# Performance work log

Hardware: AMD Instinct MI355X
Metric: run time of the kernel (lower is better)

## Reference

```python
import jax, jax.numpy as jnp
import numpy as np
from jax import lax

B, N, T, H, V, C = 256, 196, 26, 512, 12000, 1000


def setup_inputs() -> dict:
    key = jax.random.key(0)
    ks = jax.random.split(key, 24)
    g = lambda i, shape, s=0.02: jax.random.normal(ks[i], shape, jnp.float32) * s
    z = lambda *shape: jnp.zeros(shape, jnp.float32)
    return {
        "image": jax.random.normal(ks[0], (B, N, H), jnp.float32),
        "question": jax.random.randint(ks[1], (B, T), 0, V, jnp.int32),
        "embed_table": g(2, (V, H), 1.0),
        "W_img": g(3, (H, H)), "b_img": z(H),
        "W_uni": g(4, (1, H, H)), "b_uni": z(H),
        "W_bi": g(5, (2, H, H)), "b_bi": z(H),
        "W_tri": g(6, (3, H, H)), "b_tri": z(H),
        "lstm_k": g(7, (H, 4 * H)), "lstm_rk": g(8, (H, 4 * H)), "lstm_b": z(4 * H),
        "W_corr": g(9, (H, H)), "b_corr": z(H),
        "W_qe": g(10, (H, H)), "b_qe": z(H),
        "W_ie": g(11, (H, H)), "b_ie": z(H),
        "w_qa": g(12, (H, 1)), "b_qa": z(1),
        "w_ia": g(13, (H, 1)), "b_ia": z(1),
        "W_w": g(14, (H, H)), "b_w": z(H),
        "W_p": g(15, (2 * H, H)), "b_p": z(H),
        "W_s": g(16, (2 * H, H)), "b_s": z(H),
        "W_fc1": g(17, (H, 2 * H)), "b_fc1": z(2 * H),
        "W_fc": g(18, (2 * H, C)), "b_fc": z(C),
    }


def _conv1d(x, w, b, dil):
    # x: [B,T,H], w: [k, in, out] (WIO). TF 'same' padding == XLA SAME.
    y = lax.conv_general_dilated(x, w, window_strides=(1,), padding='SAME',
                                 rhs_dilation=(dil,),
                                 dimension_numbers=('NWC', 'WIO', 'NWC'))
    return y + b


def _lstm(x, k, rk, b):
    # Keras LSTM, gate order i,f,c,o; inference (dropout off).
    xp = jnp.einsum('bth,hg->btg', x, k) + b  # [B,T,4H]
    h0 = jnp.zeros((x.shape[0], rk.shape[0]), x.dtype)

    def step(carry, xt):
        h, c = carry
        zg = xt + h @ rk
        i, f, g, o = jnp.split(zg, 4, axis=-1)
        i, f, o = jax.nn.sigmoid(i), jax.nn.sigmoid(f), jax.nn.sigmoid(o)
        c = f * c + i * jnp.tanh(g)
        h = o * jnp.tanh(c)
        return (h, c), h

    _, hs = lax.scan(step, (h0, h0), jnp.swapaxes(xp, 0, 1))
    return jnp.swapaxes(hs, 0, 1)  # [B,T,H]


def _co_attention(img_feat, ques_feat, W_corr, b_corr, W_qe, b_qe, W_ie, b_ie,
                  w_qa, b_qa, w_ia, b_ia):
    img_corr = img_feat @ W_corr + b_corr                       # [B,N,H]
    wm = jnp.tanh(jnp.einsum('btd,bnd->btn', ques_feat, img_corr))  # affinity
    ques_embed = ques_feat @ W_qe + b_qe                        # [B,T,H]
    img_embed = img_feat @ W_ie + b_ie                          # [B,N,H]
    ques_sum = jnp.tanh(jnp.einsum('btn,bnd->btd', wm, img_embed) + ques_embed)
    ques_att = jax.nn.softmax((ques_sum @ w_qa + b_qa)[..., 0], axis=-1)  # [B,T]
    img_sum = jnp.tanh(jnp.einsum('btn,btd->bnd', wm, ques_embed) + img_embed)
    img_att = jax.nn.softmax((img_sum @ w_ia + b_ia)[..., 0], axis=-1)    # [B,N]
    q_feat = jnp.einsum('bt,btd->bd', ques_att, ques_feat)
    v_feat = jnp.einsum('bn,bnd->bd', img_att, img_feat)
    return v_feat, q_feat


def reference(image, question, embed_table, W_img, b_img, W_uni, b_uni, W_bi, b_bi,
              W_tri, b_tri, lstm_k, lstm_rk, lstm_b, W_corr, b_corr, W_qe, b_qe,
              W_ie, b_ie, w_qa, b_qa, w_ia, b_ia, W_w, b_w, W_p, b_p, W_s, b_s,
              W_fc1, b_fc1, W_fc, b_fc):
    img = jnp.tanh(image @ W_img + b_img)                       # [B,N,H]
    words = embed_table[question]                               # [B,T,H]
    uni = jnp.tanh(_conv1d(words, W_uni, b_uni, 1))
    bi = jnp.tanh(_conv1d(words, W_bi, b_bi, 2))
    tri = jnp.tanh(_conv1d(words, W_tri, b_tri, 2))
    phrase = jnp.tanh(jnp.maximum(jnp.maximum(uni, bi), tri))   # maxpool over 3 n-grams
    sentence = _lstm(phrase, lstm_k, lstm_rk, lstm_b)
    ca = lambda v, q: _co_attention(v, q, W_corr, b_corr, W_qe, b_qe, W_ie, b_ie,
                                    w_qa, b_qa, w_ia, b_ia)
    v_word, q_word = ca(img, words)
    v_phr, q_phr = ca(img, phrase)
    v_sent, q_sent = ca(img, sentence)
    h_w = jnp.tanh((q_word + v_word) @ W_w + b_w)
    h_p = jnp.tanh(jnp.concatenate([q_phr + v_phr, h_w], axis=1) @ W_p + b_p)
    h_s = jnp.tanh(jnp.concatenate([q_sent + v_sent, h_p], axis=1) @ W_s + b_s)
    fc1 = jax.nn.relu(h_s @ W_fc1 + b_fc1)
    return jax.nn.softmax(fc1 @ W_fc + b_fc, axis=-1)           # [B,C]
```

## Files before the change

kernel.cpp:

```cpp
#include <hip/hip_runtime.h>
#include <hip/hip_bf16.h>
#include <math.h>

#define Bq   256
#define Nimg 196
#define Tseq 26
#define Hd   512
#define H4   2048
#define Ccls 1000
#define KP   1536
#define MT3  19968

typedef int   int4v  __attribute__((ext_vector_type(4)));
typedef float f32x4  __attribute__((ext_vector_type(4)));

#define SWZ8(x) ((x) ^ (((x) >> 3) & 7))

__device__ __forceinline__ float fast_tanh(float x) {
    float e = __expf(2.0f * x);
    return 1.0f - 2.0f * __builtin_amdgcn_rcpf(e + 1.0f);
}
__device__ __forceinline__ float fast_sigmoid(float x) {
    return __builtin_amdgcn_rcpf(1.0f + __expf(-x));
}

__device__ __forceinline__ short f2bf(float x) {
    union { float f; unsigned u; } a; a.f = x;
    unsigned r = a.u + 0x7FFF + ((a.u >> 16) & 1);
    return (short)(r >> 16);
}
__device__ __forceinline__ float bf2f(short b) {
    union { float f; unsigned u; } a; a.u = ((unsigned)(unsigned short)b) << 16;
    return a.f;
}

__global__ void embed_kernel(const int* __restrict__ q, const float* __restrict__ table,
                             short* __restrict__ words2) {
    int row = blockIdx.x;
    int tok = q[row];
    int c4 = threadIdx.x * 4;
    float4 v = *reinterpret_cast<const float4*>(table + (size_t)tok * Hd + c4);
    short h0 = f2bf(v.x), h1 = f2bf(v.y), h2 = f2bf(v.z), h3 = f2bf(v.w);
    short l0 = f2bf(v.x - bf2f(h0)), l1 = f2bf(v.y - bf2f(h1));
    short l2 = f2bf(v.z - bf2f(h2)), l3 = f2bf(v.w - bf2f(h3));
    *reinterpret_cast<short4*>(words2 + (size_t)row * 1024 + c4) = make_short4(h0, h1, h2, h3);
    *reinterpret_cast<short4*>(words2 + (size_t)row * 1024 + 512 + c4) = make_short4(l0, l1, l2, l3);
}

__global__ void split_kernel(const float* __restrict__ X, short* __restrict__ X2) {
    int i4 = blockIdx.x * 256 + threadIdx.x;
    int m = i4 >> 7, c4 = (i4 & 127) * 4;
    float4 v = *reinterpret_cast<const float4*>(X + ((size_t)m << 9) + c4);
    short h0 = f2bf(v.x), h1 = f2bf(v.y), h2 = f2bf(v.z), h3 = f2bf(v.w);
    short l0 = f2bf(v.x - bf2f(h0)), l1 = f2bf(v.y - bf2f(h1));
    short l2 = f2bf(v.z - bf2f(h2)), l3 = f2bf(v.w - bf2f(h3));
    *reinterpret_cast<short4*>(X2 + (size_t)m * 1024 + c4) = make_short4(h0, h1, h2, h3);
    *reinterpret_cast<short4*>(X2 + (size_t)m * 1024 + 512 + c4) = make_short4(l0, l1, l2, l3);
}

__global__ __launch_bounds__(256) void wsplit_all_kernel(
    const float* __restrict__ W_img, const float* __restrict__ W_corr,
    const float* __restrict__ W_ie, const float* __restrict__ W_qe,
    const float* __restrict__ W_uni, const float* __restrict__ W_bi,
    const float* __restrict__ W_tri, const float* __restrict__ lstm_k,
    short* __restrict__ WimgT2, short* __restrict__ WcorrR2,
    short* __restrict__ WieT2, short* __restrict__ WqeT2,
    short* __restrict__ WconvT2, short* __restrict__ lkT2) {
    const int z = blockIdx.z;
    const int tid = threadIdx.x;
    const int k0 = blockIdx.y * 64;
    const size_t HK = (size_t)Hd * KP;
    if (z == 1) {
        const int n0 = blockIdx.x * 64;
        const int n = tid >> 2, ksub = (tid & 3) * 16;
        const float* src = W_corr + (size_t)(n0 + n) * Hd + k0 + ksub;
        size_t base = (size_t)(n0 + n) * KP + k0 + ksub;
        #pragma unroll
        for (int k = 0; k < 16; ++k) {
            float x = src[k];
            short h = f2bf(x);
            short l = f2bf(x - bf2f(h));
            WcorrR2[base + k] = h;
            WcorrR2[base + 512 + k] = h;
            WcorrR2[base + 1024 + k] = l;
        }
        return;
    }
    const float* W; short* WT2; int Nw, n0;
    if (z < 10) {
        Nw = Hd; n0 = blockIdx.x * 64;
        switch (z) {
            case 0: W = W_img;  WT2 = WimgT2;  break;
            case 2: W = W_ie;   WT2 = WieT2;   break;
            case 3: W = W_qe;   WT2 = WqeT2;   break;
            case 4: W = W_uni;                     WT2 = WconvT2 + 0 * HK; break;
            case 5: W = W_bi;                      WT2 = WconvT2 + 1 * HK; break;
            case 6: W = W_bi + (size_t)Hd * Hd;    WT2 = WconvT2 + 2 * HK; break;
            case 7: W = W_tri;                     WT2 = WconvT2 + 3 * HK; break;
            case 8: W = W_tri + (size_t)Hd * Hd;   WT2 = WconvT2 + 4 * HK; break;
            default:W = W_tri + 2 * (size_t)Hd * Hd; WT2 = WconvT2 + 5 * HK; break;
        }
    } else {
        Nw = H4; W = lstm_k; WT2 = lkT2;
        n0 = ((z - 10) * 8 + blockIdx.x) * 64;
    }
    __shared__ float tile[64][65];
    #pragma unroll
    for (int p = 0; p < 16; ++p) {
        int r = p * 4 + (tid >> 6);
        int c = tid & 63;
        tile[r][c] = W[(size_t)(k0 + r) * Nw + n0 + c];
    }
    __syncthreads();
    const int n = tid >> 2;
    const int ksub = (tid & 3) * 16;
    size_t base = (size_t)(n0 + n) * KP + k0 + ksub;
    #pragma unroll
    for (int k = 0; k < 16; ++k) {
        float x = tile[ksub + k][n];
        short h = f2bf(x);
        short l = f2bf(x - bf2f(h));
        WT2[base + k] = h;
        WT2[base + 512 + k] = h;
        WT2[base + 1024 + k] = l;
    }
}

__global__ __launch_bounds__(256) void qb_kernel(const short* __restrict__ Q2,
                                                 const float* __restrict__ b_corr,
                                                 float* __restrict__ qb) {
    const int tid = threadIdx.x, lane = tid & 63, wid = tid >> 6;
    const int r = blockIdx.x * 4 + wid;
    const short* row = Q2 + (size_t)r * 1024 + lane * 8;
    float v = 0.f;
    #pragma unroll
    for (int k = 0; k < 8; ++k) {
        float x = bf2f(row[k]) + bf2f(row[512 + k]);
        v += x * b_corr[lane * 8 + k];
    }
    #pragma unroll
    for (int off = 32; off; off >>= 1) v += __shfl_xor(v, off);
    if (lane == 0) qb[r] = v;
}

__device__ __forceinline__ void mfma16(f32x4& acc, int4v a, int4v b) {
    asm volatile("v_mfma_f32_16x16x32_bf16 %0, %1, %2, %0" : "+v"(acc) : "v"(a), "v"(b));
}

template <int ACT, int OUT>
__global__ __launch_bounds__(512) void mfma_gemm8_kernel(
    const short* __restrict__ A2, const short* __restrict__ W2T,
    const float* __restrict__ bias, float* __restrict__ C, short* __restrict__ C2,
    int M, int N) {
    __shared__ __align__(16) short L[2][2][4][4096];
    const int tid = threadIdx.x;
    const int lane = tid & 63, wid = tid >> 6;
    const int Cn = N >> 8;
    const int nwg = (M >> 8) * Cn;
    int Lb = blockIdx.x;
    int xcd = Lb & 7, lq = Lb >> 3;
    int q8 = nwg >> 3, r8 = nwg & 7;
    int logical = (xcd < r8 ? xcd * (q8 + 1) : r8 * (q8 + 1) + (xcd - r8) * q8) + lq;
    const int row0 = (logical / Cn) << 8, col0 = (logical % Cn) << 8;
    const int wm = wid >> 2, wn = wid & 3;
    const int sdec = SWZ8(tid);
    const int frs = sdec >> 6, rs = (sdec >> 2) & 15, kb = sdec & 3;
    const int koff = kb * 8;
    const int aro = frs * 16 + rs;
    const short* aptr[2]; const short* bptr[2];
    aptr[0] = A2 + (size_t)(row0 + aro) * 1024;
    aptr[1] = A2 + (size_t)(row0 + 128 + aro) * 1024;
    bptr[0] = W2T + (size_t)(col0 + aro) * KP;
    bptr[1] = W2T + (size_t)(col0 + 128 + aro) * KP;
    const int ldso = wid * 64 * 8;
    auto STAGE = [&](int slot, int tile, int p) {
        int h = p & 1, kh = p >> 1;
        int kk = tile * 64 + kh * 32 + koff;
        int ka = kk >= 1024 ? kk - 1024 : kk;
        __builtin_amdgcn_global_load_lds(
            (const __attribute__((address_space(1))) void*)(aptr[h] + ka),
            (__attribute__((address_space(3))) void*)(&L[slot][0][h * 2 + kh][ldso]),
            16, 0, 0);
        __builtin_amdgcn_global_load_lds(
            (const __attribute__((address_space(1))) void*)(bptr[h] + kk),
            (__attribute__((address_space(3))) void*)(&L[slot][1][h * 2 + kh][ldso]),
            16, 0, 0);
    };
    f32x4 acc[8][4] = {};
    #pragma unroll
    for (int p = 0; p < 4; ++p) STAGE(0, 0, p);
    const int NT = KP / 64;
    for (int t = 0; t < NT; ++t) {
        const int sl = t & 1;
        int4v bfr[4][2];
        #pragma unroll
        for (int p = 0; p < 4; ++p) {
            if (p == 0) {
                if (t + 1 < NT) {
                    STAGE(sl ^ 1, t + 1, 0);
                    asm volatile("s_waitcnt vmcnt(2)" ::: "memory");
                } else {
                    asm volatile("s_waitcnt vmcnt(0)" ::: "memory");
                }
                __builtin_amdgcn_s_barrier();
                __builtin_amdgcn_sched_barrier(0);
                #pragma unroll
                for (int nf = 0; nf < 4; ++nf)
                    #pragma unroll
                    for (int kh = 0; kh < 2; ++kh) {
                        int off = ((wn & 1) * 4 + nf) * 64 + (lane & 15) * 4 + (lane >> 4);
                        bfr[nf][kh] = *reinterpret_cast<const int4v*>(
                            &L[sl][1][(wn >> 1) * 2 + kh][SWZ8(off) * 8]);
                    }
            } else {
                if (t + 1 < NT) STAGE(sl ^ 1, t + 1, p);
            }
            int4v af[2][2];
            #pragma unroll
            for (int i = 0; i < 2; ++i)
                #pragma unroll
                for (int kh = 0; kh < 2; ++kh) {
                    int off = (p * 2 + i) * 64 + (lane & 15) * 4 + (lane >> 4);
                    af[i][kh] = *reinterpret_cast<const int4v*>(
                        &L[sl][0][wm * 2 + kh][SWZ8(off) * 8]);
                }
            __builtin_amdgcn_s_setprio(1);
            #pragma unroll
            for (int i = 0; i < 2; ++i)
                #pragma unroll
                for (int nf = 0; nf < 4; ++nf)
                    #pragma unroll
                    for (int kh = 0; kh < 2; ++kh)
                        mfma16(acc[p * 2 + i][nf], af[i][kh], bfr[nf][kh]);
            __builtin_amdgcn_s_setprio(0);
        }
        asm volatile("s_waitcnt lgkmcnt(0)" ::: "memory");
        __builtin_amdgcn_s_barrier();
        __builtin_amdgcn_sched_barrier(0);
    }
    asm volatile("s_nop 7\n\ts_nop 7" ::: "memory");
    #pragma unroll
    for (int mf = 0; mf < 8; ++mf) {
        #pragma unroll
        for (int nf = 0; nf < 4; ++nf) {
            int col = col0 + wn * 64 + nf * 16 + (lane & 15);
            float bv;
            if (OUT == 2) bv = (col >= 512) ? bias[col - 512] : 0.f;
            else bv = bias ? bias[col] : 0.f;
            #pragma unroll
            for (int r = 0; r < 4; ++r) {
                int row = row0 + wm * 128 + mf * 16 + (lane >> 4) * 4 + r;
                float v = acc[mf][nf][r] + bv;
                if (ACT == 1) v = fast_tanh(v);
                if (OUT == 0) {
                    C[(size_t)row * N + col] = v;
                } else if (OUT == 1) {
                    short h = f2bf(v), l = f2bf(v - bf2f(h));
                    C2[(size_t)row * 1024 + col] = h;
                    C2[(size_t)row * 1024 + 512 + col] = l;
                } else {
                    if (col < 512) {
                        short h = f2bf(v), l = f2bf(v - bf2f(h));
                        C2[(size_t)row * 1024 + col] = h;
                        C2[(size_t)row * 1024 + 512 + col] = l;
                    } else {
                        C[(size_t)row * Hd + (col - 512)] = v;
                    }
                }
            }
        }
    }
}

__global__ __launch_bounds__(256) void wm3_mfma_kernel(
    const short* __restrict__ Qc2, const short* __restrict__ img2,
    const float* __restrict__ qb, float* __restrict__ wm0, float* __restrict__ wm1,
    float* __restrict__ wm2) {
    __shared__ __align__(16) short Asl[2][4096];
    __shared__ __align__(16) short Bsl[2][4096];
    const int tid = threadIdx.x;
    const int lane = tid & 63, wid = tid >> 6;
    const int col0 = blockIdx.x * 128;
    const int b = blockIdx.y;
    const int wmq = wid >> 1, wn = wid & 1;
    const short* ab[2]; const short* bb[2]; int koff[2];
    #pragma unroll
    for (int c = 0; c < 2; ++c) {
        int d = c * 256 + tid;
        int s = SWZ8(d);
        int fr = s >> 6, r = (s >> 2) & 15, kb = s & 3;
        koff[c] = kb * 8;
        int arow = fr * 16 + r;
        int lvl = arow / 26, at = arow - lvl * 26;
        if (arow >= 78) { lvl = 0; at = 0; }
        ab[c] = Qc2 + ((size_t)lvl * (Bq * Tseq) + (size_t)(b * 26 + at)) * 1024;
        int brow = col0 + fr * 16 + r;
        if (brow > 195) brow = 195;
        bb[c] = img2 + ((size_t)(b * 196 + brow)) * 1024;
    }
    auto STAGE = [&](int buf, int k0) {
        #pragma unroll
        for (int c = 0; c < 2; ++c) {
            int kk = k0 + koff[c];
            int ka = kk >= 1024 ? kk - 1024 : kk;
            int kbv = kk >= 512 ? kk - 512 : kk;
            __builtin_amdgcn_global_load_lds(
                (const __attribute__((address_space(1))) void*)(ab[c] + ka),
                (__attribute__((address_space(3))) void*)(&Asl[buf][(c * 256 + wid * 64) * 8]),
                16, 0, 0);
            __builtin_amdgcn_global_load_lds(
                (const __attribute__((address_space(1))) void*)(bb[c] + kbv),
                (__attribute__((address_space(3))) void*)(&Bsl[buf][(c * 256 + wid * 64) * 8]),
                16, 0, 0);
        }
    };
    f32x4 acc[4][4] = {};
    STAGE(0, 0);
    int cur = 0;
    for (int k0 = 0; k0 < KP; k0 += 32) {
        if (k0 + 32 < KP) {
            STAGE(cur ^ 1, k0 + 32);
            asm volatile("s_waitcnt vmcnt(4)" ::: "memory");
        } else {
            asm volatile("s_waitcnt vmcnt(0)" ::: "memory");
        }
        __builtin_amdgcn_s_barrier();
        __builtin_amdgcn_sched_barrier(0);
        int4v af[4], bfr[4];
        #pragma unroll
        for (int f = 0; f < 4; ++f) {
            int sa = (wmq * 4 + f) * 64 + (lane & 15) * 4 + (lane >> 4);
            af[f] = *reinterpret_cast<const int4v*>(&Asl[cur][SWZ8(sa) * 8]);
            int sb = (wn * 4 + f) * 64 + (lane & 15) * 4 + (lane >> 4);
            bfr[f] = *reinterpret_cast<const int4v*>(&Bsl[cur][SWZ8(sb) * 8]);
        }
        #pragma unroll
        for (int i = 0; i < 4; ++i)
            #pragma unroll
            for (int j = 0; j < 4; ++j)
                mfma16(acc[i][j], af[i], bfr[j]);
        asm volatile("s_waitcnt lgkmcnt(0)" ::: "memory");
        __builtin_amdgcn_s_barrier();
        __builtin_amdgcn_sched_barrier(0);
        cur ^= 1;
    }
    asm volatile("s_nop 7\n\ts_nop 7" ::: "memory");
    #pragma unroll
    for (int i = 0; i < 4; ++i) {
        #pragma unroll
        for (int j = 0; j < 4; ++j) {
            int col = col0 + wn * 64 + j * 16 + (lane & 15);
            if (col >= Nimg) continue;
            #pragma unroll
            for (int r = 0; r < 4; ++r) {
                int row = wmq * 64 + i * 16 + (lane >> 4) * 4 + r;
                if (row >= 78) continue;
                int lvl = row / 26, t = row - lvl * 26;
                float* dst = (lvl == 0) ? wm0 : (lvl == 1) ? wm1 : wm2;
                float qbv = qb[(size_t)lvl * (Bq * Tseq) + b * 26 + t];
                dst[((size_t)(b * 26 + t)) * Nimg + col] = fast_tanh(acc[i][j][r] + qbv);
            }
        }
    }
}

__global__ void conv_combine_kernel(const float* __restrict__ Y,
                                    const float* __restrict__ bu, const float* __restrict__ bb,
                                    const float* __restrict__ bt,
                                    short* __restrict__ phrase2) {
    int idx = blockIdx.x * 256 + threadIdx.x;
    int m = idx >> 9, c = idx & 511;
    int t = m % Tseq;
    const float* Ym = Y + (size_t)m * 3072;
    float u = Ym[c] + bu[c];
    float bv = bb[c];
    if (t > 0)  bv += Ym[-3072 + 512 + c];
    if (t < 25) bv += Ym[3072 + 1024 + c];
    float tv = Ym[2048 + c] + bt[c];
    if (t > 1)  tv += Ym[-6144 + 1536 + c];
    if (t < 24) tv += Ym[6144 + 2560 + c];
    float ph = fast_tanh(fmaxf(fmaxf(fast_tanh(u), fast_tanh(bv)), fast_tanh(tv)));
    short h = f2bf(ph), l = f2bf(ph - bf2f(h));
    phrase2[(size_t)m * 1024 + c] = h;
    phrase2[(size_t)m * 1024 + 512 + c] = l;
}

template <int ACT>
__global__ __launch_bounds__(256) void gemm_kernel(
    const float* __restrict__ A, int lda,
    const float* __restrict__ W, int ldw,
    const float* __restrict__ bias,
    float* __restrict__ C, int ldc,
    int M, int Ncols, int K) {
    __shared__ float As[16][68];
    __shared__ float Ws[16][68];
    const int tid = threadIdx.x;
    const int tx4 = (tid & 15) * 4, ty4 = (tid >> 4) * 4;
    const int row0 = blockIdx.y * 64, col0 = blockIdx.x * 64;
    const int am = tid >> 2, ak = (tid & 3) * 4;
    const int wk = tid >> 4, wc = (tid & 15) * 4;
    float acc[4][4] = {};
    for (int k0 = 0; k0 < K; k0 += 16) {
        {
            int gr = row0 + am;
            float4 v = make_float4(0.f, 0.f, 0.f, 0.f);
            if (gr < M) v = *reinterpret_cast<const float4*>(A + (size_t)gr * lda + k0 + ak);
            As[ak + 0][am] = v.x; As[ak + 1][am] = v.y; As[ak + 2][am] = v.z; As[ak + 3][am] = v.w;
        }
        {
            int gc = col0 + wc;
            const float* wp = W + (size_t)(k0 + wk) * ldw + gc;
            float4 v = make_float4(0.f, 0.f, 0.f, 0.f);
            if (gc + 3 < Ncols) v = *reinterpret_cast<const float4*>(wp);
            else {
                if (gc + 0 < Ncols) v.x = wp[0];
                if (gc + 1 < Ncols) v.y = wp[1];
                if (gc + 2 < Ncols) v.z = wp[2];
                if (gc + 3 < Ncols) v.w = wp[3];
            }
            Ws[wk][wc + 0] = v.x; Ws[wk][wc + 1] = v.y; Ws[wk][wc + 2] = v.z; Ws[wk][wc + 3] = v.w;
        }
        __syncthreads();
        #pragma unroll 4
        for (int kk = 0; kk < 16; ++kk) {
            float4 a4 = *reinterpret_cast<const float4*>(&As[kk][ty4]);
            float4 b4 = *reinterpret_cast<const float4*>(&Ws[kk][tx4]);
            float a[4] = {a4.x, a4.y, a4.z, a4.w};
            float b[4] = {b4.x, b4.y, b4.z, b4.w};
            #pragma unroll
            for (int i = 0; i < 4; ++i)
                #pragma unroll
                for (int j = 0; j < 4; ++j) acc[i][j] += a[i] * b[j];
        }
        __syncthreads();
    }
    #pragma unroll
    for (int i = 0; i < 4; ++i) {
        int r = row0 + ty4 + i;
        if (r >= M) continue;
        #pragma unroll
        for (int j = 0; j < 4; ++j) {
            int c = col0 + tx4 + j;
            if (c >= Ncols) continue;
            float v = acc[i][j];
            if (bias) v += bias[c];
            if (ACT == 1) v = fast_tanh(v);
            else if (ACT == 2) v = fmaxf(v, 0.f);
            C[(size_t)r * ldc + c] = v;
        }
    }
}

__global__ __launch_bounds__(256) void lstm_gemm_kernel(
    const float* __restrict__ h, const float* __restrict__ rk, float* __restrict__ zgp) {
    __shared__ float As[16][68];
    __shared__ float Ws[16][68];
    const int tid = threadIdx.x;
    const int tx4 = (tid & 15) * 4, ty4 = (tid >> 4) * 4;
    const int col0 = blockIdx.x * 64, row0 = blockIdx.y * 64, kb = blockIdx.z * 256;
    const int am = tid >> 2, ak = (tid & 3) * 4;
    const int wk = tid >> 4, wc = (tid & 15) * 4;
    float acc[4][4] = {};
    for (int k0 = kb; k0 < kb + 256; k0 += 16) {
        {
            float4 v = *reinterpret_cast<const float4*>(h + (size_t)(row0 + am) * Hd + k0 + ak);
            As[ak + 0][am] = v.x; As[ak + 1][am] = v.y; As[ak + 2][am] = v.z; As[ak + 3][am] = v.w;
        }
        {
            *reinterpret_cast<float4*>(&Ws[wk][wc]) =
                *reinterpret_cast<const float4*>(rk + (size_t)(k0 + wk) * H4 + col0 + wc);
        }
        __syncthreads();
        #pragma unroll 4
        for (int kk = 0; kk < 16; ++kk) {
            float4 a4 = *reinterpret_cast<const float4*>(&As[kk][ty4]);
            float4 b4 = *reinterpret_cast<const float4*>(&Ws[kk][tx4]);
            float a[4] = {a4.x, a4.y, a4.z, a4.w};
            float b[4] = {b4.x, b4.y, b4.z, b4.w};
            #pragma unroll
            for (int i = 0; i < 4; ++i)
                #pragma unroll
                for (int j = 0; j < 4; ++j) acc[i][j] += a[i] * b[j];
        }
        __syncthreads();
    }
    float* dst = zgp + (size_t)blockIdx.z * (Bq * H4);
    #pragma unroll
    for (int i = 0; i < 4; ++i) {
        int r = row0 + ty4 + i;
        *reinterpret_cast<float4*>(dst + (size_t)r * H4 + col0 + tx4) =
            make_float4(acc[i][0], acc[i][1], acc[i][2], acc[i][3]);
    }
}

__global__ __launch_bounds__(256) void lstm_gates_kernel(
    const float* __restrict__ zgp, const float* __restrict__ xp,
    float* __restrict__ c, float* __restrict__ h, short* __restrict__ sent2, int t) {
    int i = blockIdx.x * 256 + threadIdx.x;
    int b = i >> 9, hh = i & 511;
    const float* xr = xp + ((size_t)b * Tseq + t) * H4;
    float z[4];
    #pragma unroll
    for (int g = 0; g < 4; ++g) {
        float s = xr[g * 512 + hh];
        #pragma unroll
        for (int kc = 0; kc < 2; ++kc)
            s += zgp[(size_t)kc * (Bq * H4) + (size_t)b * H4 + g * 512 + hh];
        z[g] = s;
    }
    float ig = fast_sigmoid(z[0]);
    float fg = fast_sigmoid(z[1]);
    float gg = fast_tanh(z[2]);
    float og = fast_sigmoid(z[3]);
    float cv = fg * c[i] + ig * gg;
    c[i] = cv;
    float hv = og * fast_tanh(cv);
    h[i] = hv;
    short hb = f2bf(hv), lb = f2bf(hv - bf2f(hb));
    sent2[((size_t)b * Tseq + t) * 1024 + hh] = hb;
    sent2[((size_t)b * Tseq + t) * 1024 + 512 + hh] = lb;
}

__global__ __launch_bounds__(256) void qlog3_kernel(
    const float* __restrict__ wm0, const float* __restrict__ wm1, const float* __restrict__ wm2,
    const float* __restrict__ Ie, const float* __restrict__ qe0, const float* __restrict__ qe1,
    const float* __restrict__ qe2, const float* __restrict__ wqa, float* __restrict__ qlogp) {
    const int b = blockIdx.x, chunk = blockIdx.y;
    __shared__ float wms[3][Tseq][Nimg];
    __shared__ float red[4][40];
    const int tid = threadIdx.x;
    const float* wsrc[3] = {wm0, wm1, wm2};
    for (int e = tid; e < 3 * 1274; e += 256) {
        int c = e / 1274, r = e % 1274;
        *reinterpret_cast<float4*>(&wms[c][0][0] + 4 * r) =
            *reinterpret_cast<const float4*>(wsrc[c] + (size_t)b * (Tseq * Nimg) + 4 * r);
    }
    __syncthreads();
    const int hl = tid & 127, thalf = tid >> 7, tt0 = thalf * 13;
    const int h1 = chunk * 256 + hl, h2 = h1 + 128;
    float acc[3][13][2] = {};
    const float* iep1 = Ie + (size_t)b * Nimg * Hd + h1;
    const float* iep2 = Ie + (size_t)b * Nimg * Hd + h2;
    for (int n4 = 0; n4 < 49; ++n4) {
        float ieA0 = iep1[(size_t)(4 * n4 + 0) * Hd];
        float ieA1 = iep1[(size_t)(4 * n4 + 1) * Hd];
        float ieA2 = iep1[(size_t)(4 * n4 + 2) * Hd];
        float ieA3 = iep1[(size_t)(4 * n4 + 3) * Hd];
        float ieB0 = iep2[(size_t)(4 * n4 + 0) * Hd];
        float ieB1 = iep2[(size_t)(4 * n4 + 1) * Hd];
        float ieB2 = iep2[(size_t)(4 * n4 + 2) * Hd];
        float ieB3 = iep2[(size_t)(4 * n4 + 3) * Hd];
        #pragma unroll
        for (int c = 0; c < 3; ++c)
            #pragma unroll
            for (int tt = 0; tt < 13; ++tt) {
                float4 w4 = *reinterpret_cast<const float4*>(&wms[c][tt0 + tt][4 * n4]);
                acc[c][tt][0] += w4.x * ieA0 + w4.y * ieA1 + w4.z * ieA2 + w4.w * ieA3;
                acc[c][tt][1] += w4.x * ieB0 + w4.y * ieB1 + w4.z * ieB2 + w4.w * ieB3;
            }
    }
    const float wq1 = wqa[h1], wq2 = wqa[h2];
    const int lane = tid & 63, w = tid >> 6;
    const float* qes[3] = {qe0, qe1, qe2};
    #pragma unroll
    for (int c = 0; c < 3; ++c)
        #pragma unroll
        for (int tt = 0; tt < 13; ++tt) {
            int t = tt0 + tt;
            const float* qrow = qes[c] + ((size_t)(b * 26 + t)) * Hd;
            float v = fast_tanh(acc[c][tt][0] + qrow[h1]) * wq1 +
                      fast_tanh(acc[c][tt][1] + qrow[h2]) * wq2;
            #pragma unroll
            for (int off = 32; off; off >>= 1) v += __shfl_xor(v, off);
            if (lane == 0) red[w][c * 13 + tt] = v;
        }
    __syncthreads();
    if (tid < 39) {
        int c = tid / 13, tt = tid % 13;
        qlogp[((size_t)c * Bq + b) * (2 * 26) + chunk * 26 + tt] = red[0][tid] + red[1][tid];
    } else if (tid >= 64 && tid < 103) {
        int id = tid - 64;
        int c = id / 13, tt = id % 13;
        qlogp[((size_t)c * Bq + b) * (2 * 26) + chunk * 26 + 13 + tt] = red[2][id] + red[3][id];
    }
}

__global__ __launch_bounds__(256) void ilog3_kernel(
    const float* __restrict__ wmb, const float* __restrict__ qeb,
    const float* __restrict__ Ie, const float* __restrict__ wia,
    float* __restrict__ ilogp) {
    const int b = blockIdx.x, lvl = blockIdx.z;
    const int nbase = (blockIdx.y & 1) * 98, hc = blockIdx.y >> 1;
    const int hbase = hc * 256;
    const float* wm = wmb + (size_t)lvl * Bq * Tseq * Nimg;
    const float* qe = qeb + (size_t)lvl * Bq * Tseq * Hd;
    float* ilog = ilogp + (size_t)hc * (3 * Bq * Nimg) + (size_t)lvl * Bq * Nimg;
    __shared__ float qes[Tseq][260];
    __shared__ __align__(16) float wms[Tseq][104];
    const int tid = threadIdx.x;
    for (int e = tid; e < Tseq * 64; e += 256) {
        int t = e >> 6, q4 = (e & 63) * 4;
        *reinterpret_cast<float4*>(&qes[t][q4]) =
            *reinterpret_cast<const float4*>(qe + ((size_t)(b * 26 + t)) * Hd + hbase + q4);
    }
    for (int e = tid; e < Tseq * 100; e += 256) {
        int t = e / 100, n = e % 100;
        wms[t][n] = (n < 98 && nbase + n < Nimg)
                    ? wm[((size_t)(b * 26 + t)) * Nimg + nbase + n] : 0.f;
    }
    __syncthreads();
    const int lane = tid & 63, w = tid >> 6;
    const int nw0 = w * 4;
    float4 wi = *reinterpret_cast<const float4*>(wia + hbase + 4 * lane);
    auto PASS = [&](int gbeg, int NG) {
        float4 acc[4][4];
        #pragma unroll
        for (int g = 0; g < 4; ++g)
            #pragma unroll
            for (int i = 0; i < 4; ++i) acc[g][i] = make_float4(0.f, 0.f, 0.f, 0.f);
        for (int t = 0; t < Tseq; ++t) {
            float4 q0 = *reinterpret_cast<const float4*>(&qes[t][4 * lane]);
            #pragma unroll
            for (int g = 0; g < 4; ++g) {
                if (g >= NG) continue;
                int n0 = nw0 + (gbeg + g) * 16;
                if (n0 < 98) {
                    float4 wv = *reinterpret_cast<const float4*>(&wms[t][n0]);
                    float wvv[4] = {wv.x, wv.y, wv.z, wv.w};
                    #pragma unroll
                    for (int i = 0; i < 4; ++i) {
                        acc[g][i].x += wvv[i] * q0.x; acc[g][i].y += wvv[i] * q0.y;
                        acc[g][i].z += wvv[i] * q0.z; acc[g][i].w += wvv[i] * q0.w;
                    }
                }
            }
        }
        #pragma unroll
        for (int g = 0; g < 4; ++g) {
            if (g >= NG) continue;
            int n0 = nw0 + (gbeg + g) * 16;
            if (n0 >= 98) continue;
            #pragma unroll
            for (int i = 0; i < 4; ++i) {
                int n = n0 + i;
                if (n >= 98 || nbase + n >= Nimg) continue;
                const float* iebn = Ie + ((size_t)(b * Nimg) + nbase + n) * Hd + hbase;
                float4 e0 = *reinterpret_cast<const float4*>(iebn + 4 * lane);
                float v = fast_tanh(acc[g][i].x + e0.x) * wi.x +
                          fast_tanh(acc[g][i].y + e0.y) * wi.y +
                          fast_tanh(acc[g][i].z + e0.z) * wi.z +
                          fast_tanh(acc[g][i].w + e0.w) * wi.w;
                #pragma unroll
                for (int off = 32; off; off >>= 1) v += __shfl_xor(v, off);
                if (lane == 0) ilog[(size_t)b * Nimg + nbase + n] = v;
            }
        }
    };
    PASS(0, 4);
    PASS(4, 3);
}

__global__ void softmaxT_part_kernel(const float* __restrict__ lgp, float* __restrict__ att) {
    int b = blockIdx.x, c = blockIdx.y, lane = threadIdx.x;
    float v = -INFINITY;
    if (lane < Tseq) {
        const float* p = lgp + ((size_t)c * Bq + b) * (2 * 26) + lane;
        v = p[0] + p[26];
    }
    float m = v;
    #pragma unroll
    for (int off = 32; off; off >>= 1) m = fmaxf(m, __shfl_xor(m, off));
    float e = (lane < Tseq) ? __expf(v - m) : 0.f;
    float s = e;
    #pragma unroll
    for (int off = 32; off; off >>= 1) s += __shfl_xor(s, off);
    if (lane < Tseq) att[((size_t)c * Bq + b) * Tseq + lane] = e / s;
}

__global__ void softmax_N_kernel(const float* __restrict__ lg, float* __restrict__ att) {
    int b = blockIdx.x, c = blockIdx.y, lane = threadIdx.x;
    const float* lb0 = lg + ((size_t)c * Bq + b) * Nimg;
    const float* lb1 = lb0 + (size_t)3 * Bq * Nimg;
    float* ab = att + ((size_t)c * Bq + b) * Nimg;
    float v[4]; float m = -INFINITY;
    #pragma unroll
    for (int k = 0; k < 4; ++k) {
        int n = lane + 64 * k;
        v[k] = (n < Nimg) ? (lb0[n] + lb1[n]) : -INFINITY;
        m = fmaxf(m, v[k]);
    }
    #pragma unroll
    for (int off = 32; off; off >>= 1) m = fmaxf(m, __shfl_xor(m, off));
    float e[4]; float s = 0.f;
    #pragma unroll
    for (int k = 0; k < 4; ++k) {
        int n = lane + 64 * k;
        e[k] = (n < Nimg) ? __expf(v[k] - m) : 0.f;
        s += e[k];
    }
    #pragma unroll
    for (int off = 32; off; off >>= 1) s += __shfl_xor(s, off);
    #pragma unroll
    for (int k = 0; k < 4; ++k) {
        int n = lane + 64 * k;
        if (n < Nimg) ab[n] = e[k] / s;
    }
}

__global__ __launch_bounds__(256) void feat3_kernel(
    const float* __restrict__ qatt0, const float* __restrict__ qatt1, const float* __restrict__ qatt2,
    const float* __restrict__ iatt0, const float* __restrict__ iatt1, const float* __restrict__ iatt2,
    const short* __restrict__ Qw2, const short* __restrict__ Qp2, const short* __restrict__ Qs2,
    const short* __restrict__ img2, float* __restrict__ s_part) {
    const int b = blockIdx.x, chunk = blockIdx.y, tid = threadIdx.x;
    float a[3][2] = {};
    if (chunk == 0) {
        for (int t = 0; t < Tseq; ++t) {
            float w0 = qatt0[b * Tseq + t], w1 = qatt1[b * Tseq + t], w2 = qatt2[b * Tseq + t];
            const short* p0 = Qw2 + ((size_t)(b * Tseq + t)) * 1024;
            const short* p1 = Qp2 + ((size_t)(b * Tseq + t)) * 1024;
            const short* p2 = Qs2 + ((size_t)(b * Tseq + t)) * 1024;
            a[0][0] += w0 * (bf2f(p0[tid]) + bf2f(p0[512 + tid]));
            a[0][1] += w0 * (bf2f(p0[256 + tid]) + bf2f(p0[768 + tid]));
            a[1][0] += w1 * (bf2f(p1[tid]) + bf2f(p1[512 + tid]));
            a[1][1] += w1 * (bf2f(p1[256 + tid]) + bf2f(p1[768 + tid]));
            a[2][0] += w2 * (bf2f(p2[tid]) + bf2f(p2[512 + tid]));
            a[2][1] += w2 * (bf2f(p2[256 + tid]) + bf2f(p2[768 + tid]));
        }
    }
    int ns, ne;
    if (chunk == 0)      { ns = 0;   ne = 30;  }
    else if (chunk == 1) { ns = 30;  ne = 86;  }
    else if (chunk == 2) { ns = 86;  ne = 141; }
    else                 { ns = 141; ne = 196; }
    for (int n = ns; n < ne; ++n) {
        float w0 = iatt0[b * Nimg + n], w1 = iatt1[b * Nimg + n], w2 = iatt2[b * Nimg + n];
        const short* p = img2 + ((size_t)(b * Nimg) + n) * 1024;
        float v0 = bf2f(p[tid]) + bf2f(p[512 + tid]);
        float v1 = bf2f(p[256 + tid]) + bf2f(p[768 + tid]);
        a[0][0] += w0 * v0; a[0][1] += w0 * v1;
        a[1][0] += w1 * v0; a[1][1] += w1 * v1;
        a[2][0] += w2 * v0; a[2][1] += w2 * v1;
    }
    #pragma unroll
    for (int c = 0; c < 3; ++c) {
        float* dst = s_part + ((size_t)(chunk * 3 + c) * Bq + b) * Hd;
        dst[tid] = a[c][0];
        dst[tid + 256] = a[c][1];
    }
}

__global__ void feat_combine_kernel(const float* __restrict__ s_part, float* __restrict__ s0,
                                    float* __restrict__ s1, float* __restrict__ s2) {
    int i = blockIdx.x * 256 + threadIdx.x;
    int c = i / (Bq * Hd), r = i % (Bq * Hd);
    float v = 0.f;
    #pragma unroll
    for (int ch = 0; ch < 4; ++ch) v += s_part[(size_t)(ch * 3 + c) * (Bq * Hd) + r];
    float* dst = (c == 0) ? s0 : (c == 1) ? s1 : s2;
    dst[r] = v;
}

__global__ void concat_kernel(const float* __restrict__ x, const float* __restrict__ y,
                              float* __restrict__ out) {
    int i = blockIdx.x * 256 + threadIdx.x;
    int b = i >> 9, j = i & 511;
    out[(size_t)b * 1024 + j] = x[i];
    out[(size_t)b * 1024 + 512 + j] = y[i];
}

__global__ __launch_bounds__(256) void softmax_C_kernel(const float* __restrict__ lg,
                                                        float* __restrict__ out) {
    int b = blockIdx.x, tid = threadIdx.x;
    __shared__ float red[4];
    const float* lb = lg + (size_t)b * Ccls;
    float v[4]; float m = -INFINITY;
    #pragma unroll
    for (int k = 0; k < 4; ++k) {
        int j = tid + 256 * k;
        v[k] = (j < Ccls) ? lb[j] : -INFINITY;
        m = fmaxf(m, v[k]);
    }
    #pragma unroll
    for (int off = 32; off; off >>= 1) m = fmaxf(m, __shfl_xor(m, off));
    int lane = tid & 63, w = tid >> 6;
    if (lane == 0) red[w] = m;
    __syncthreads();
    m = fmaxf(fmaxf(red[0], red[1]), fmaxf(red[2], red[3]));
    __syncthreads();
    float e[4]; float s = 0.f;
    #pragma unroll
    for (int k = 0; k < 4; ++k) {
        int j = tid + 256 * k;
        e[k] = (j < Ccls) ? __expf(v[k] - m) : 0.f;
        s += e[k];
    }
    #pragma unroll
    for (int off = 32; off; off >>= 1) s += __shfl_xor(s, off);
    if (lane == 0) red[w] = s;
    __syncthreads();
    s = red[0] + red[1] + red[2] + red[3];
    float inv = 1.f / s;
    #pragma unroll
    for (int k = 0; k < 4; ++k) {
        int j = tid + 256 * k;
        if (j < Ccls) out[(size_t)b * Ccls + j] = e[k] * inv;
    }
}

extern "C" void kernel_launch(void* const* d_in, const int* in_sizes, int n_in,
                              void* d_out, int out_size, void* d_ws, size_t ws_size,
                              hipStream_t stream) {
    const float* image   = (const float*)d_in[0];
    const int*   question= (const int*)  d_in[1];
    const float* embed   = (const float*)d_in[2];
    const float* W_img   = (const float*)d_in[3];
    const float* b_img   = (const float*)d_in[4];
    const float* W_uni   = (const float*)d_in[5];
    const float* b_uni   = (const float*)d_in[6];
    const float* W_bi    = (const float*)d_in[7];
    const float* b_bi    = (const float*)d_in[8];
    const float* W_tri   = (const float*)d_in[9];
    const float* b_tri   = (const float*)d_in[10];
    const float* lstm_k  = (const float*)d_in[11];
    const float* lstm_rk = (const float*)d_in[12];
    const float* lstm_b  = (const float*)d_in[13];
    const float* W_corr  = (const float*)d_in[14];
    const float* b_corr  = (const float*)d_in[15];
    const float* W_qe    = (const float*)d_in[16];
    const float* b_qe    = (const float*)d_in[17];
    const float* W_ie    = (const float*)d_in[18];
    const float* b_ie    = (const float*)d_in[19];
    const float* w_qa    = (const float*)d_in[20];
    const float* w_ia    = (const float*)d_in[22];
    const float* W_w     = (const float*)d_in[24];
    const float* b_w     = (const float*)d_in[25];
    const float* W_p     = (const float*)d_in[26];
    const float* b_p     = (const float*)d_in[27];
    const float* W_s     = (const float*)d_in[28];
    const float* b_s     = (const float*)d_in[29];
    const float* W_fc1   = (const float*)d_in[30];
    const float* b_fc1   = (const float*)d_in[31];
    const float* W_fc    = (const float*)d_in[32];
    const float* b_fc    = (const float*)d_in[33];

    float* p = (float*)d_ws;
    size_t off = 0;
    auto take = [&](size_t n) { float* r = p + off; off += n; return r; };
    auto take_s = [&](size_t n) { short* r = (short*)(p + off); off += n / 2; return r; };
    float* bufB   = take((size_t)Bq * Nimg * Hd);
    float* xp     = take((size_t)Bq * Tseq * H4);
    float* wm0    = take((size_t)Bq * Tseq * Nimg);
    float* wm1    = take((size_t)Bq * Tseq * Nimg);
    float* wm2    = take((size_t)Bq * Tseq * Nimg);
    float* hbuf   = take((size_t)Bq * Hd);
    float* cbuf   = take((size_t)Bq * Hd);
    float* zgp    = take((size_t)2 * Bq * H4);
    float* qlogp  = take((size_t)3 * Bq * 4 * Tseq);
    float* qatt0  = take((size_t)Bq * Tseq);
    float* qatt1  = take((size_t)Bq * Tseq);
    float* qatt2  = take((size_t)Bq * Tseq);
    float* ilogp  = take((size_t)2 * 3 * Bq * Nimg);
    float* iatt0  = take((size_t)Bq * Nimg);
    float* iatt1  = take((size_t)Bq * Nimg);
    float* iatt2  = take((size_t)Bq * Nimg);
    float* qb     = take((size_t)MT3);
    short* imgS2   = take_s((size_t)Bq * Nimg * 1024);
    short* words2  = take_s((size_t)Bq * Tseq * 1024);
    short* phrase2 = take_s((size_t)Bq * Tseq * 1024);
    short* sentn2  = take_s((size_t)Bq * Tseq * 1024);
    short* WimgT2  = take_s((size_t)Hd * KP);
    short* WieT2   = take_s((size_t)Hd * KP);
    short* WcorrR2 = take_s((size_t)Hd * KP);
    short* WqeT2   = take_s((size_t)Hd * KP);
    short* WconvT2 = take_s((size_t)6 * Hd * KP);
    short* lkT2    = take_s((size_t)H4 * KP);

    float* qe0 = xp;
    float* qe1 = xp + (size_t)Bq * Tseq * Hd;
    float* qe2 = xp + 2 * (size_t)Bq * Tseq * Hd;
    float* s_part = xp + 3 * (size_t)Bq * Tseq * Hd;
    float* Y      = bufB;
    short* image2 = (short*)bufB;
    short* Qc2    = (short*)bufB;
    float* catb   = wm0;
    float* fc1b   = wm0 + (size_t)Bq * 2 * Hd;
    float* logits = wm0 + 2 * (size_t)Bq * 2 * Hd;
    float* s0     = wm1;
    float* s1     = wm1 + 1 * (size_t)Bq * Hd;
    float* s2     = wm1 + 2 * (size_t)Bq * Hd;
    float* hw     = wm1 + 3 * (size_t)Bq * Hd;
    float* hp     = wm1 + 4 * (size_t)Bq * Hd;
    float* hsv    = wm1 + 5 * (size_t)Bq * Hd;

    const int MI = Bq * Nimg;
    const int MT = Bq * Tseq;

    wsplit_all_kernel<<<dim3(8, 8, 14), 256, 0, stream>>>(
        W_img, W_corr, W_ie, W_qe, W_uni, W_bi, W_tri, lstm_k,
        WimgT2, WcorrR2, WieT2, WqeT2, WconvT2, lkT2);

    embed_kernel<<<MT, 128, 0, stream>>>(question, embed, words2);
    split_kernel<<<MI / 2, 256, 0, stream>>>(image, image2);
    mfma_gemm8_kernel<1, 1><<<dim3((MI / 256) * (Hd / 256)), 512, 0, stream>>>(
        image2, WimgT2, b_img, nullptr, imgS2, MI, Hd);
    mfma_gemm8_kernel<0, 0><<<dim3((MT / 256) * (3072 / 256)), 512, 0, stream>>>(
        words2, WconvT2, nullptr, Y, nullptr, MT, 3072);
    conv_combine_kernel<<<(MT * Hd) / 256, 256, 0, stream>>>(Y, b_uni, b_bi, b_tri, phrase2);
    mfma_gemm8_kernel<0, 0><<<dim3((MT / 256) * (H4 / 256)), 512, 0, stream>>>(
        phrase2, lkT2, lstm_b, xp, nullptr, MT, H4);
    hipMemsetAsync(hbuf, 0, (size_t)Bq * Hd * sizeof(float), stream);
    hipMemsetAsync(cbuf, 0, (size_t)Bq * Hd * sizeof(float), stream);
    for (int t = 0; t < Tseq; ++t) {
        lstm_gemm_kernel<<<dim3(32, 4, 2), 256, 0, stream>>>(hbuf, lstm_rk, zgp);
        lstm_gates_kernel<<<(Bq * Hd) / 256, 256, 0, stream>>>(zgp, xp, cbuf, hbuf, sentn2, t);
    }
    qb_kernel<<<MT3 / 4, 256, 0, stream>>>(words2, b_corr, qb);
    mfma_gemm8_kernel<0, 2><<<dim3((MT3 / 256) * (1024 / 256)), 512, 0, stream>>>(
        words2, WcorrR2, b_qe, qe0, Qc2, MT3, 1024);
    wm3_mfma_kernel<<<dim3(2, Bq), 256, 0, stream>>>(Qc2, imgS2, qb, wm0, wm1, wm2);
    mfma_gemm8_kernel<0, 0><<<dim3((MI / 256) * (Hd / 256)), 512, 0, stream>>>(
        imgS2, WieT2, b_ie, bufB, nullptr, MI, Hd);
    qlog3_kernel<<<dim3(Bq, 2), 256, 0, stream>>>(wm0, wm1, wm2, bufB, qe0, qe1, qe2, w_qa, qlogp);
    softmaxT_part_kernel<<<dim3(Bq, 3), 64, 0, stream>>>(qlogp, qatt0);
    ilog3_kernel<<<dim3(Bq, 4, 3), 256, 0, stream>>>(wm0, qe0, bufB, w_ia, ilogp);
    softmax_N_kernel<<<dim3(Bq, 3), 64, 0, stream>>>(ilogp, iatt0);
    feat3_kernel<<<dim3(Bq, 4), 256, 0, stream>>>(qatt0, qatt1, qatt2, iatt0, iatt1, iatt2,
                                                  words2, phrase2, sentn2, imgS2, s_part);
    feat_combine_kernel<<<(3 * Bq * Hd) / 256, 256, 0, stream>>>(s_part, s0, s1, s2);
    gemm_kernel<1><<<dim3(Hd / 64, Bq / 64), 256, 0, stream>>>(
        s0, Hd, W_w, Hd, b_w, hw, Hd, Bq, Hd, Hd);
    concat_kernel<<<(Bq * Hd) / 256, 256, 0, stream>>>(s1, hw, catb);
    gemm_kernel<1><<<dim3(Hd / 64, Bq / 64), 256, 0, stream>>>(
        catb, 2 * Hd, W_p, Hd, b_p, hp, Hd, Bq, Hd, 2 * Hd);
    concat_kernel<<<(Bq * Hd) / 256, 256, 0, stream>>>(s2, hp, catb);
    gemm_kernel<1><<<dim3(Hd / 64, Bq / 64), 256, 0, stream>>>(
        catb, 2 * Hd, W_s, Hd, b_s, hsv, Hd, Bq, Hd, 2 * Hd);
    gemm_kernel<2><<<dim3((2 * Hd) / 64, Bq / 64), 256, 0, stream>>>(
        hsv, Hd, W_fc1, 2 * Hd, b_fc1, fc1b, 2 * Hd, Bq, 2 * Hd, Hd);
    gemm_kernel<0><<<dim3((Ccls + 63) / 64, Bq / 64), 256, 0, stream>>>(
        fc1b, 2 * Hd, W_fc, Ccls, b_fc, logits, Ccls, Bq, Ccls, 2 * Hd);
    softmax_C_kernel<<<Bq, 256, 0, stream>>>(logits, (float*)d_out);
}
```

Before: 1.789 ms.

## Merge correlation and image-embedding GEMMs into one dual-problem launch

```diff
diff --git a/kernel.cpp b/kernel.cpp
--- a/kernel.cpp
+++ b/kernel.cpp
@@ -272,6 +272,135 @@
     }
 }
 
+__global__ __launch_bounds__(512) void mfma_gemm8_dual_kernel(
+    const short* __restrict__ A0, const short* __restrict__ W0,
+    const float* __restrict__ bias0, float* __restrict__ C0, short* __restrict__ C20,
+    int M0, int N0, int nwg0,
+    const short* __restrict__ A1, const short* __restrict__ W1,
+    const float* __restrict__ bias1, float* __restrict__ C1,
+    int M1, int N1) {
+    __shared__ __align__(16) short L[2][2][4][4096];
+    const int tid = threadIdx.x;
+    const int lane = tid & 63, wid = tid >> 6;
+    const short* A2; const short* W2T; const float* bias; float* C; short* C2;
+    int N, OUT, nwg, Lb;
+    if ((int)blockIdx.x < nwg0) {
+        A2 = A0; W2T = W0; bias = bias0; C = C0; C2 = C20;
+        N = N0; OUT = 2; nwg = nwg0; Lb = blockIdx.x;
+    } else {
+        A2 = A1; W2T = W1; bias = bias1; C = C1; C2 = nullptr;
+        N = N1; OUT = 0; nwg = (M1 >> 8) * (N1 >> 8); Lb = blockIdx.x - nwg0;
+    }
+    const int Cn = N >> 8;
+    int xcd = Lb & 7, lq = Lb >> 3;
+    int q8 = nwg >> 3, r8 = nwg & 7;
+    int logical = (xcd < r8 ? xcd * (q8 + 1) : r8 * (q8 + 1) + (xcd - r8) * q8) + lq;
+    const int row0 = (logical / Cn) << 8, col0 = (logical % Cn) << 8;
+    const int wm = wid >> 2, wn = wid & 3;
+    const int sdec = SWZ8(tid);
+    const int frs = sdec >> 6, rs = (sdec >> 2) & 15, kb = sdec & 3;
+    const int koff = kb * 8;
+    const int aro = frs * 16 + rs;
+    const short* aptr[2]; const short* bptr[2];
+    aptr[0] = A2 + (size_t)(row0 + aro) * 1024;
+    aptr[1] = A2 + (size_t)(row0 + 128 + aro) * 1024;
+    bptr[0] = W2T + (size_t)(col0 + aro) * KP;
+    bptr[1] = W2T + (size_t)(col0 + 128 + aro) * KP;
+    const int ldso = wid * 64 * 8;
+    auto STAGE = [&](int slot, int tile, int p) {
+        int h = p & 1, kh = p >> 1;
+        int kk = tile * 64 + kh * 32 + koff;
+        int ka = kk >= 1024 ? kk - 1024 : kk;
+        __builtin_amdgcn_global_load_lds(
+            (const __attribute__((address_space(1))) void*)(aptr[h] + ka),
+            (__attribute__((address_space(3))) void*)(&L[slot][0][h * 2 + kh][ldso]),
+            16, 0, 0);
+        __builtin_amdgcn_global_load_lds(
+            (const __attribute__((address_space(1))) void*)(bptr[h] + kk),
+            (__attribute__((address_space(3))) void*)(&L[slot][1][h * 2 + kh][ldso]),
+            16, 0, 0);
+    };
+    f32x4 acc[8][4] = {};
+    #pragma unroll
+    for (int p = 0; p < 4; ++p) STAGE(0, 0, p);
+    const int NT = KP / 64;
+    for (int t = 0; t < NT; ++t) {
+        const int sl = t & 1;
+        int4v bfr[4][2];
+        #pragma unroll
+        for (int p = 0; p < 4; ++p) {
+            if (p == 0) {
+                if (t + 1 < NT) {
+                    STAGE(sl ^ 1, t + 1, 0);
+                    asm volatile("s_waitcnt vmcnt(2)" ::: "memory");
+                } else {
+                    asm volatile("s_waitcnt vmcnt(0)" ::: "memory");
+                }
+                __builtin_amdgcn_s_barrier();
+                __builtin_amdgcn_sched_barrier(0);
+                #pragma unroll
+                for (int nf = 0; nf < 4; ++nf)
+                    #pragma unroll
+                    for (int kh = 0; kh < 2; ++kh) {
+                        int off = ((wn & 1) * 4 + nf) * 64 + (lane & 15) * 4 + (lane >> 4);
+                        bfr[nf][kh] = *reinterpret_cast<const int4v*>(
+                            &L[sl][1][(wn >> 1) * 2 + kh][SWZ8(off) * 8]);
+                    }
+            } else {
+                if (t + 1 < NT) STAGE(sl ^ 1, t + 1, p);
+            }
+            int4v af[2][2];
+            #pragma unroll
+            for (int i = 0; i < 2; ++i)
+                #pragma unroll
+                for (int kh = 0; kh < 2; ++kh) {
+                    int off = (p * 2 + i) * 64 + (lane & 15) * 4 + (lane >> 4);
+                    af[i][kh] = *reinterpret_cast<const int4v*>(
+                        &L[sl][0][wm * 2 + kh][SWZ8(off) * 8]);
+                }
+            __builtin_amdgcn_s_setprio(1);
+            #pragma unroll
+            for (int i = 0; i < 2; ++i)
+                #pragma unroll
+                for (int nf = 0; nf < 4; ++nf)
+                    #pragma unroll
+                    for (int kh = 0; kh < 2; ++kh)
+                        mfma16(acc[p * 2 + i][nf], af[i][kh], bfr[nf][kh]);
+            __builtin_amdgcn_s_setprio(0);
+        }
+        asm volatile("s_waitcnt lgkmcnt(0)" ::: "memory");
+        __builtin_amdgcn_s_barrier();
+        __builtin_amdgcn_sched_barrier(0);
+    }
+    asm volatile("s_nop 7\n\ts_nop 7" ::: "memory");
+    #pragma unroll
+    for (int mf = 0; mf < 8; ++mf) {
+        #pragma unroll
+        for (int nf = 0; nf < 4; ++nf) {
+            int col = col0 + wn * 64 + nf * 16 + (lane & 15);
+            float bv;
+            if (OUT == 2) bv = (col >= 512) ? bias[col - 512] : 0.f;
+            else bv = bias[col];
+            #pragma unroll
+            for (int r = 0; r < 4; ++r) {
+                int row = row0 + wm * 128 + mf * 16 + (lane >> 4) * 4 + r;
+                float v = acc[mf][nf][r] + bv;
+                if (OUT == 0) {
+                    C[(size_t)row * N + col] = v;
+                } else {
+                    if (col < 512) {
+                        short h = f2bf(v), l = f2bf(v - bf2f(h));
+                        C2[(size_t)row * 1024 + col] = h;
+                        C2[(size_t)row * 1024 + 512 + col] = l;
+                    } else {
+                        C[(size_t)row * Hd + (col - 512)] = v;
+                    }
+                }
+            }
+        }
+    }
+}
+
 __global__ __launch_bounds__(256) void wm3_mfma_kernel(
     const short* __restrict__ Qc2, const short* __restrict__ img2,
     const float* __restrict__ qb, float* __restrict__ wm0, float* __restrict__ wm1,
@@ -869,6 +998,7 @@
     short* words2  = take_s((size_t)Bq * Tseq * 1024);
     short* phrase2 = take_s((size_t)Bq * Tseq * 1024);
     short* sentn2  = take_s((size_t)Bq * Tseq * 1024);
+    short* Qc2     = take_s((size_t)MT3 * 1024);
     short* WimgT2  = take_s((size_t)Hd * KP);
     short* WieT2   = take_s((size_t)Hd * KP);
     short* WcorrR2 = take_s((size_t)Hd * KP);
@@ -882,7 +1012,6 @@
     float* s_part = xp + 3 * (size_t)Bq * Tseq * Hd;
     float* Y      = bufB;
     short* image2 = (short*)bufB;
-    short* Qc2    = (short*)bufB;
     float* catb   = wm0;
     float* fc1b   = wm0 + (size_t)Bq * 2 * Hd;
     float* logits = wm0 + 2 * (size_t)Bq * 2 * Hd;
@@ -916,11 +1045,14 @@
         lstm_gates_kernel<<<(Bq * Hd) / 256, 256, 0, stream>>>(zgp, xp, cbuf, hbuf, sentn2, t);
     }
     qb_kernel<<<MT3 / 4, 256, 0, stream>>>(words2, b_corr, qb);
-    mfma_gemm8_kernel<0, 2><<<dim3((MT3 / 256) * (1024 / 256)), 512, 0, stream>>>(
-        words2, WcorrR2, b_qe, qe0, Qc2, MT3, 1024);
+    {
+        const int nwg0 = (MT3 / 256) * (1024 / 256);
+        const int nwg1 = (MI / 256) * (Hd / 256);
+        mfma_gemm8_dual_kernel<<<dim3(nwg0 + nwg1), 512, 0, stream>>>(
+            words2, WcorrR2, b_qe, qe0, Qc2, MT3, 1024, nwg0,
+            imgS2, WieT2, b_ie, bufB, MI, Hd);
+    }
     wm3_mfma_kernel<<<dim3(2, Bq), 256, 0, stream>>>(Qc2, imgS2, qb, wm0, wm1, wm2);
-    mfma_gemm8_kernel<0, 0><<<dim3((MI / 256) * (Hd / 256)), 512, 0, stream>>>(
-        imgS2, WieT2, b_ie, bufB, nullptr, MI, Hd);
     qlog3_kernel<<<dim3(Bq, 2), 256, 0, stream>>>(wm0, wm1, wm2, bufB, qe0, qe1, qe2, w_qa, qlogp);
     softmaxT_part_kernel<<<dim3(Bq, 3), 64, 0, stream>>>(qlogp, qatt0);
     ilog3_kernel<<<dim3(Bq, 4, 3), 256, 0, stream>>>(wm0, qe0, bufB, w_ia, ilogp);
```

After: 1.763 ms. No clear change (-1.4%).
